# Kernel tuning notes

Measured on AMD Instinct MI355X. Metric: run time of the kernel, lower is better.

## Reference

```python
import jax, jax.numpy as jnp
import numpy as np

N = 50000
E = 800000
IN_CH = 128
HID = 64
HEADS = 4
EPS = 1e-5
NEG_SLOPE = 0.2


def _gat_conv(x, src, dst, W, a_src, a_dst, b, heads, out_ch, concat):
    n = x.shape[0]
    h = (x @ W).reshape(n, heads, out_ch)                      # [N,H,C]
    alpha_src = jnp.sum(h * a_src, axis=-1)                    # [N,H]
    alpha_dst = jnp.sum(h * a_dst, axis=-1)                    # [N,H]
    e = jax.nn.leaky_relu(alpha_src[src] + alpha_dst[dst], NEG_SLOPE)  # [E',H]
    # segment softmax over incoming edges of each destination node
    m = jax.ops.segment_max(e, dst, num_segments=n)            # [N,H]
    e = jnp.exp(e - m[dst])
    denom = jax.ops.segment_sum(e, dst, num_segments=n)        # [N,H]
    alpha = e / denom[dst]                                     # [E',H]
    msg = h[src] * alpha[:, :, None]                           # [E',H,C]
    out = jax.ops.segment_sum(msg, dst, num_segments=n)        # [N,H,C]
    if concat:
        out = out.reshape(n, heads * out_ch)
    else:
        out = out.mean(axis=1)
    return out + b


def _bn_eval(x, gamma, beta, mean, var):
    return (x - mean) * (gamma / jnp.sqrt(var + EPS)) + beta


def setup_inputs() -> dict:
    key = jax.random.key(0)
    ks = jax.random.split(key, 24)
    s = 0.1
    x = jax.random.normal(ks[0], (N, IN_CH), dtype=jnp.float32)
    edge_index = jax.random.randint(ks[1], (2, E), 0, N, dtype=jnp.int32)
    d0, d1 = IN_CH, HID * HEADS
    inp = {
        'x': x, 'edge_index': edge_index,
        # layer 0: in_ch -> hidden, heads=4, concat
        'W0': jax.random.normal(ks[2], (d0, HEADS * HID), jnp.float32) * s,
        'as0': jax.random.normal(ks[3], (HEADS, HID), jnp.float32) * s,
        'ad0': jax.random.normal(ks[4], (HEADS, HID), jnp.float32) * s,
        'b0': jax.random.normal(ks[5], (HEADS * HID,), jnp.float32) * s,
        # layer 1: hidden*heads -> hidden, heads=4, concat
        'W1': jax.random.normal(ks[6], (d1, HEADS * HID), jnp.float32) * s,
        'as1': jax.random.normal(ks[7], (HEADS, HID), jnp.float32) * s,
        'ad1': jax.random.normal(ks[8], (HEADS, HID), jnp.float32) * s,
        'b1': jax.random.normal(ks[9], (HEADS * HID,), jnp.float32) * s,
        # layer 2: hidden*heads -> 1, heads=1, no concat
        'W2': jax.random.normal(ks[10], (d1, 1), jnp.float32) * s,
        'as2': jax.random.normal(ks[11], (1, 1), jnp.float32) * s,
        'ad2': jax.random.normal(ks[12], (1, 1), jnp.float32) * s,
        'b2': jax.random.normal(ks[13], (1,), jnp.float32) * s,
        # batchnorm (eval) params for the two hidden layers
        'g0': jnp.ones((d1,), jnp.float32),
        'be0': jnp.zeros((d1,), jnp.float32),
        'm0': jax.random.normal(ks[14], (d1,), jnp.float32) * s,
        'v0': jnp.ones((d1,), jnp.float32),
        'g1': jnp.ones((d1,), jnp.float32),
        'be1': jnp.zeros((d1,), jnp.float32),
        'm1': jax.random.normal(ks[15], (d1,), jnp.float32) * s,
        'v1': jnp.ones((d1,), jnp.float32),
    }
    return inp


def reference(x, edge_index, W0, as0, ad0, b0, W1, as1, ad1, b1,
              W2, as2, ad2, b2, g0, be0, m0, v0, g1, be1, m1, v1):
    n = x.shape[0]
    loops = jnp.arange(n, dtype=edge_index.dtype)
    src = jnp.concatenate([edge_index[0], loops])  # add self-loops (PyG default)
    dst = jnp.concatenate([edge_index[1], loops])

    # layer 0 (no residual: shapes differ)
    h = _gat_conv(x, src, dst, W0, as0, ad0, b0, HEADS, HID, True)
    h = jax.nn.elu(_bn_eval(h, g0, be0, m0, v0))

    # layer 1 (residual: shapes match)
    res = h
    h = _gat_conv(h, src, dst, W1, as1, ad1, b1, HEADS, HID, True)
    h = jax.nn.elu(_bn_eval(h, g1, be1, m1, v1)) + res

    # output layer: heads=1, concat=False -> [N,1]
    out = _gat_conv(h, src, dst, W2, as2, ad2, b2, 1, 1, False)
    return out.squeeze(-1)
```

## Files before the change

### kernel.cpp

```cpp
#include <hip/hip_runtime.h>
#include <math.h>

#define NEG_SLOPE 0.2f
#define BN_EPS 1e-5f

typedef __attribute__((ext_vector_type(8))) short bf16x8;
typedef __attribute__((ext_vector_type(4))) float f32x4;

static __device__ __forceinline__ unsigned short f2bf(float f){
    unsigned u = __float_as_uint(f);
    u += 0x7FFFu + ((u >> 16) & 1u);
    return (unsigned short)(u >> 16);
}
static __device__ __forceinline__ float bf2f(unsigned short v){
    return __uint_as_float((unsigned)v << 16);
}

static __device__ __forceinline__ void gload_lds16(const void* g, void* l){
    __builtin_amdgcn_global_load_lds(
        (const __attribute__((address_space(1))) void*)g,
        (__attribute__((address_space(3))) void*)l, 16, 0, 0);
}

__global__ void conv_hilo_kernel(const float* __restrict__ x,
                                 unsigned short* __restrict__ hi,
                                 unsigned short* __restrict__ lo, int n4)
{
    int i = blockIdx.x * 256 + threadIdx.x;
    if (i >= n4) return;
    const float4 v = ((const float4*)x)[i];
    ushort4 h4, l4;
    h4.x = f2bf(v.x); l4.x = f2bf(v.x - bf2f(h4.x));
    h4.y = f2bf(v.y); l4.y = f2bf(v.y - bf2f(h4.y));
    h4.z = f2bf(v.z); l4.z = f2bf(v.z - bf2f(h4.z));
    h4.w = f2bf(v.w); l4.w = f2bf(v.w - bf2f(h4.w));
    ((ushort4*)hi)[i] = h4; ((ushort4*)lo)[i] = l4;
}

__global__ void repack_w_kernel(const float* __restrict__ W,
                                unsigned short* __restrict__ wbhi,
                                unsigned short* __restrict__ wblo)
{
    const int o = blockIdx.x * 256 + threadIdx.x;
    const int j = o & 7, ln = (o >> 3) & 63, ct = (o >> 9) & 15, kt = o >> 13;
    const int k = kt * 32 + 8 * (ln >> 4) + j;
    const int col = ct * 16 + (ln & 15);
    const float v = W[k * 256 + col];
    const unsigned short hb = f2bf(v);
    wbhi[o] = hb; wblo[o] = f2bf(v - bf2f(hb));
}

template<int K>
__global__ __launch_bounds__(256) void mfma_gemm_alpha(
    const unsigned short* __restrict__ xhi, const unsigned short* __restrict__ xlo,
    const unsigned short* __restrict__ wbhi, const unsigned short* __restrict__ wblo,
    const float* __restrict__ a_s, const float* __restrict__ a_d,
    unsigned short* __restrict__ hout,
    float* __restrict__ asrc, float* __restrict__ adst, int N)
{
    __shared__ unsigned short xa[8][512];
    __shared__ unsigned short wb[32][512];
    const int t = threadIdx.x, lane = t & 63, wid = t >> 6;
    const int n0 = blockIdx.x * 64;

    f32x4 acc[4][4];
#pragma unroll
    for (int rt = 0; rt < 4; ++rt)
#pragma unroll
        for (int q = 0; q < 4; ++q) acc[rt][q] = (f32x4){0.f, 0.f, 0.f, 0.f};

    for (int kt = 0; kt < K / 32; ++kt){
        __syncthreads();
#pragma unroll
        for (int ii = 0; ii < 2; ++ii){
            const int i = wid * 2 + ii;
            const int rt = i >> 1, plane = i & 1;
            int node = n0 + rt * 16 + (lane & 15);
            if (node > N - 1) node = N - 1;
            const unsigned short* src = (plane ? xlo : xhi)
                + (size_t)node * K + kt * 32 + 8 * (lane >> 4);
            gload_lds16(src, &xa[i][0]);
        }
#pragma unroll
        for (int ii = 0; ii < 8; ++ii){
            const int i = wid * 8 + ii;
            const int ct = i >> 1, plane = i & 1;
            const unsigned short* base = plane ? wblo : wbhi;
            gload_lds16(base + ((size_t)(kt * 16 + ct) * 64 + lane) * 8, &wb[i][0]);
        }
        __syncthreads();

        bf16x8 a[4][2];
#pragma unroll
        for (int rt = 0; rt < 4; ++rt)
#pragma unroll
            for (int pl = 0; pl < 2; ++pl)
                a[rt][pl] = *(const bf16x8*)&xa[rt * 2 + pl][lane * 8];

#pragma unroll
        for (int q = 0; q < 4; ++q){
            const int cti = wid * 4 + q;
            const bf16x8 bhi = *(const bf16x8*)&wb[cti * 2 + 0][lane * 8];
            const bf16x8 blo = *(const bf16x8*)&wb[cti * 2 + 1][lane * 8];
#pragma unroll
            for (int rt = 0; rt < 4; ++rt){
                acc[rt][q] = __builtin_amdgcn_mfma_f32_16x16x32_bf16(a[rt][0], bhi, acc[rt][q], 0, 0, 0);
                acc[rt][q] = __builtin_amdgcn_mfma_f32_16x16x32_bf16(a[rt][1], bhi, acc[rt][q], 0, 0, 0);
                acc[rt][q] = __builtin_amdgcn_mfma_f32_16x16x32_bf16(a[rt][0], blo, acc[rt][q], 0, 0, 0);
            }
        }
    }

    const int l15 = lane & 15, lg = lane >> 4;
    float avs[4], avd[4];
#pragma unroll
    for (int q = 0; q < 4; ++q){
        avs[q] = a_s[wid * 64 + q * 16 + l15];
        avd[q] = a_d[wid * 64 + q * 16 + l15];
    }
    float sp[4][4], dp[4][4];
#pragma unroll
    for (int rt = 0; rt < 4; ++rt){
#pragma unroll
        for (int reg = 0; reg < 4; ++reg){
            const int node = n0 + rt * 16 + lg * 4 + reg;
            float s = 0.f, d = 0.f;
            unsigned short hv[4];
#pragma unroll
            for (int q = 0; q < 4; ++q){
                const float v = acc[rt][q][reg];
                s = fmaf(v, avs[q], s); d = fmaf(v, avd[q], d);
                hv[q] = f2bf(v);
            }
            if (node < N){
#pragma unroll
                for (int q = 0; q < 4; ++q)
                    hout[(size_t)node * 256 + (wid * 4 + q) * 16 + l15] = hv[q];
            }
            sp[rt][reg] = s; dp[rt][reg] = d;
        }
    }
#pragma unroll
    for (int off = 1; off <= 8; off <<= 1){
#pragma unroll
        for (int rt = 0; rt < 4; ++rt)
#pragma unroll
            for (int reg = 0; reg < 4; ++reg){
                sp[rt][reg] += __shfl_xor(sp[rt][reg], off, 64);
                dp[rt][reg] += __shfl_xor(dp[rt][reg], off, 64);
            }
    }
    if (l15 == 0){
#pragma unroll
        for (int rt = 0; rt < 4; ++rt)
#pragma unroll
            for (int reg = 0; reg < 4; ++reg){
                const int node = n0 + rt * 16 + lg * 4 + reg;
                if (node < N){
                    asrc[(size_t)node * 4 + wid] = sp[rt][reg];
                    adst[(size_t)node * 4 + wid] = dp[rt][reg];
                }
            }
    }
}

__global__ void deg_init_kernel(int* __restrict__ deg, int N){
    int i = blockIdx.x * blockDim.x + threadIdx.x;
    if (i < N) deg[i] = 1;
}

__global__ void deg_hist_kernel(const int* __restrict__ ei, int E, int* __restrict__ deg){
    int e = blockIdx.x * blockDim.x + threadIdx.x;
    if (e < E) atomicAdd(&deg[ei[E + e]], 1);
}

__global__ __launch_bounds__(256) void part_sum_kernel(const int* __restrict__ deg,
                                                       int* __restrict__ bsum, int N)
{
    __shared__ int red[256];
    const int t = threadIdx.x;
    const int i0 = blockIdx.x * 1024 + t * 4;
    int s = 0;
    if (i0 + 3 < N){
        const int4 v = *(const int4*)&deg[i0];
        s = v.x + v.y + v.z + v.w;
    } else {
#pragma unroll
        for (int j = 0; j < 4; ++j) if (i0 + j < N) s += deg[i0 + j];
    }
    red[t] = s; __syncthreads();
    for (int off = 128; off >= 1; off >>= 1){
        if (t < off) red[t] += red[t + off];
        __syncthreads();
    }
    if (t == 0) bsum[blockIdx.x] = red[0];
}

__global__ __launch_bounds__(256) void scan_part_kernel(int* __restrict__ bsum, int nb,
                                                        int* __restrict__ row, int N)
{
    __shared__ int sh[256];
    const int t = threadIdx.x;
    const int v = (t < nb) ? bsum[t] : 0;
    sh[t] = v; __syncthreads();
    for (int off = 1; off < 256; off <<= 1){
        int u = (t >= off) ? sh[t - off] : 0;
        __syncthreads();
        sh[t] += u;
        __syncthreads();
    }
    if (t < nb) bsum[t] = sh[t] - v;
    if (t == nb - 1) row[N] = sh[t];
}

__global__ __launch_bounds__(256) void distribute_kernel(const int* __restrict__ deg,
    const int* __restrict__ bsum, int* __restrict__ row, int* __restrict__ cursor, int N)
{
    __shared__ int ts[256];
    const int t = threadIdx.x;
    const int i0 = blockIdx.x * 1024 + t * 4;
    int d[4]; int s = 0;
#pragma unroll
    for (int j = 0; j < 4; ++j){ d[j] = (i0 + j < N) ? deg[i0 + j] : 0; s += d[j]; }
    ts[t] = s; __syncthreads();
    for (int off = 1; off < 256; off <<= 1){
        int u = (t >= off) ? ts[t - off] : 0;
        __syncthreads();
        ts[t] += u;
        __syncthreads();
    }
    int base = bsum[blockIdx.x] + ts[t] - s;
#pragma unroll
    for (int j = 0; j < 4; ++j){
        if (i0 + j < N){ row[i0 + j] = base; cursor[i0 + j] = base; base += d[j]; }
    }
}

__global__ void scatter_kernel(const int* __restrict__ ei, int E, int N,
                               int* __restrict__ cursor, int* __restrict__ csr)
{
    int e = blockIdx.x * blockDim.x + threadIdx.x;
    if (e >= E + N) return;
    int s, d;
    if (e < E){ s = ei[e]; d = ei[E + e]; } else { s = d = e - E; }
    int pos = atomicAdd(&cursor[d], 1);
    csr[pos] = s;
}

#define DEG_CAP 128
__global__ __launch_bounds__(256) void agg4_kernel(
    const int* __restrict__ row, const int* __restrict__ csr,
    const float* __restrict__ asrc, const float* __restrict__ adst,
    const unsigned short* __restrict__ h,
    const float* __restrict__ b, const float* __restrict__ g,
    const float* __restrict__ be, const float* __restrict__ mean,
    const float* __restrict__ var,
    const unsigned short* __restrict__ reshi, const unsigned short* __restrict__ reslo,
    unsigned short* __restrict__ outhi, unsigned short* __restrict__ outlo, int N)
{
    __shared__ float4 plds[4][DEG_CAP];
    __shared__ int    slds[4][DEG_CAP];
    const int wid = threadIdx.x >> 6, lane = threadIdx.x & 63;
    const int node = blockIdx.x * 4 + wid;
    if (node >= N) return;
    const int beg = row[node], end = row[node + 1];
    const int head = lane >> 4, l15 = lane & 15;

    const float4 ad = *(const float4*)&adst[(size_t)node * 4];

    float d0 = 0.f, d1 = 0.f, d2 = 0.f, d3 = 0.f;
    for (int i = beg + lane; i < end; i += 64){
        const int s = csr[i];
        const float4 as = *(const float4*)&asrc[(size_t)s * 4];
        float v0 = as.x + ad.x, v1 = as.y + ad.y, v2 = as.z + ad.z, v3 = as.w + ad.w;
        v0 = v0 > 0.f ? v0 : NEG_SLOPE * v0;
        v1 = v1 > 0.f ? v1 : NEG_SLOPE * v1;
        v2 = v2 > 0.f ? v2 : NEG_SLOPE * v2;
        v3 = v3 > 0.f ? v3 : NEG_SLOPE * v3;
        const float p0 = __expf(v0), p1 = __expf(v1);
        const float p2 = __expf(v2), p3 = __expf(v3);
        d0 += p0; d1 += p1; d2 += p2; d3 += p3;
        const int slot = i - beg;
        if (slot < DEG_CAP){
            plds[wid][slot] = make_float4(p0, p1, p2, p3);
            slds[wid][slot] = s;
        }
    }
    for (int off = 32; off >= 1; off >>= 1){
        d0 += __shfl_xor(d0, off, 64); d1 += __shfl_xor(d1, off, 64);
        d2 += __shfl_xor(d2, off, 64); d3 += __shfl_xor(d3, off, 64);
    }

    float a0 = 0.f, a1 = 0.f, a2 = 0.f, a3 = 0.f;
    const int deg = end - beg;
    const int degc = deg < DEG_CAP ? deg : DEG_CAP;
    const float* pbase = (const float*)&plds[wid][0];

#define EDGE_BODY(slot)                                                        \
    {                                                                          \
        const float p_ = pbase[(slot) * 4 + head];                             \
        const int s_ = slds[wid][slot];                                        \
        const ushort4 hv_ = *(const ushort4*)&h[(size_t)s_ * 256 + lane * 4];  \
        a0 = fmaf(p_, bf2f(hv_.x), a0); a1 = fmaf(p_, bf2f(hv_.y), a1);        \
        a2 = fmaf(p_, bf2f(hv_.z), a2); a3 = fmaf(p_, bf2f(hv_.w), a3);        \
    }

    int i = 0;
    for (; i + 4 <= degc; i += 4){
        EDGE_BODY(i); EDGE_BODY(i + 1); EDGE_BODY(i + 2); EDGE_BODY(i + 3);
    }
    for (; i < degc; ++i) EDGE_BODY(i);
#undef EDGE_BODY

    for (int jj = beg + DEG_CAP; jj < end; ++jj){
        const int s = csr[jj];
        const float4 as = *(const float4*)&asrc[(size_t)s * 4];
        float e0 = as.x + ad.x, e1 = as.y + ad.y, e2 = as.z + ad.z, e3 = as.w + ad.w;
        float eh = (head == 0) ? e0 : (head == 1) ? e1 : (head == 2) ? e2 : e3;
        eh = eh > 0.f ? eh : NEG_SLOPE * eh;
        const float p = __expf(eh);
        const ushort4 hv = *(const ushort4*)&h[(size_t)s * 256 + lane * 4];
        a0 = fmaf(p, bf2f(hv.x), a0); a1 = fmaf(p, bf2f(hv.y), a1);
        a2 = fmaf(p, bf2f(hv.z), a2); a3 = fmaf(p, bf2f(hv.w), a3);
    }

    const float dsel = (head == 0) ? d0 : (head == 1) ? d1 : (head == 2) ? d2 : d3;
    const float rdi = 1.f / dsel;
    const int c0 = head * 64 + 4 * l15;
    const float4 bv  = *(const float4*)&b[c0];
    const float4 gv  = *(const float4*)&g[c0];
    const float4 bev = *(const float4*)&be[c0];
    const float4 mv  = *(const float4*)&mean[c0];
    const float4 vv4 = *(const float4*)&var[c0];
    const float ava[4]  = {a0, a1, a2, a3};
    const float bva[4]  = {bv.x, bv.y, bv.z, bv.w};
    const float gva[4]  = {gv.x, gv.y, gv.z, gv.w};
    const float beva[4] = {bev.x, bev.y, bev.z, bev.w};
    const float mva[4]  = {mv.x, mv.y, mv.z, mv.w};
    const float vva[4]  = {vv4.x, vv4.y, vv4.z, vv4.w};
    float rh[4] = {0.f, 0.f, 0.f, 0.f};
    if (reshi){
        const ushort4 r1 = *(const ushort4*)&reshi[(size_t)node * 256 + c0];
        const ushort4 r2 = *(const ushort4*)&reslo[(size_t)node * 256 + c0];
        rh[0] = bf2f(r1.x) + bf2f(r2.x); rh[1] = bf2f(r1.y) + bf2f(r2.y);
        rh[2] = bf2f(r1.z) + bf2f(r2.z); rh[3] = bf2f(r1.w) + bf2f(r2.w);
    }
    unsigned short hos[4], los[4];
#pragma unroll
    for (int j = 0; j < 4; ++j){
        float vvv = ava[j] * rdi + bva[j];
        vvv = (vvv - mva[j]) * (gva[j] * rsqrtf(vva[j] + BN_EPS)) + beva[j];
        vvv = vvv > 0.f ? vvv : (__expf(vvv) - 1.f);
        vvv += rh[j];
        const unsigned short hb = f2bf(vvv);
        hos[j] = hb; los[j] = f2bf(vvv - bf2f(hb));
    }
    ushort4 ho, lo4;
    ho.x = hos[0];  ho.y = hos[1];  ho.z = hos[2];  ho.w = hos[3];
    lo4.x = los[0]; lo4.y = los[1]; lo4.z = los[2]; lo4.w = los[3];
    *(ushort4*)&outhi[(size_t)node * 256 + c0] = ho;
    *(ushort4*)&outlo[(size_t)node * 256 + c0] = lo4;
}

__global__ __launch_bounds__(256) void gemm2_kernel(
    const unsigned short* __restrict__ xhi, const unsigned short* __restrict__ xlo,
    const float* __restrict__ W2, float* __restrict__ h2, int N)
{
    const int wid = threadIdx.x >> 6, lane = threadIdx.x & 63;
    const int n = blockIdx.x * 4 + wid;
    if (n >= N) return;
    float sum = 0.f;
#pragma unroll
    for (int i = 0; i < 4; ++i){
        const int c = i * 64 + lane;
        sum += (bf2f(xhi[(size_t)n * 256 + c]) + bf2f(xlo[(size_t)n * 256 + c])) * W2[c];
    }
    for (int off = 32; off >= 1; off >>= 1) sum += __shfl_xor(sum, off, 64);
    if (lane == 0) h2[n] = sum;
}

__global__ void agg2_kernel(const int* __restrict__ row, const int* __restrict__ csr,
                            const float* __restrict__ h2,
                            const float* __restrict__ as2, const float* __restrict__ ad2,
                            const float* __restrict__ b2, float* __restrict__ out, int N)
{
    const int n = blockIdx.x * blockDim.x + threadIdx.x;
    if (n >= N) return;
    const float A_s = as2[0];
    const float hd  = h2[n] * ad2[0];
    const int beg = row[n], end = row[n + 1];
    float den = 0.f, acc = 0.f;
    for (int i = beg; i < end; ++i){
        const float hv = h2[csr[i]];
        float a = fmaf(A_s, hv, hd);
        a = a > 0.f ? a : NEG_SLOPE * a;
        const float p = __expf(a);
        den += p; acc = fmaf(p, hv, acc);
    }
    out[n] = acc / den + b2[0];
}

extern "C" void kernel_launch(void* const* d_in, const int* in_sizes, int n_in,
                              void* d_out, int out_size, void* d_ws, size_t ws_size,
                              hipStream_t stream)
{
    const float* x   = (const float*)d_in[0];
    const int*   ei  = (const int*)  d_in[1];
    const float* W0  = (const float*)d_in[2];
    const float* as0 = (const float*)d_in[3];
    const float* ad0 = (const float*)d_in[4];
    const float* b0  = (const float*)d_in[5];
    const float* W1  = (const float*)d_in[6];
    const float* as1 = (const float*)d_in[7];
    const float* ad1 = (const float*)d_in[8];
    const float* b1  = (const float*)d_in[9];
    const float* W2  = (const float*)d_in[10];
    const float* as2 = (const float*)d_in[11];
    const float* ad2 = (const float*)d_in[12];
    const float* b2  = (const float*)d_in[13];
    const float* g0  = (const float*)d_in[14];
    const float* be0 = (const float*)d_in[15];
    const float* m0  = (const float*)d_in[16];
    const float* v0  = (const float*)d_in[17];
    const float* g1  = (const float*)d_in[18];
    const float* be1 = (const float*)d_in[19];
    const float* m1  = (const float*)d_in[20];
    const float* v1  = (const float*)d_in[21];

    const int N = in_sizes[0] / 128;
    const int E = in_sizes[1] / 2;
    const int EN = E + N;

    char* w = (char*)d_ws;
    unsigned short* H    = (unsigned short*)w;  w += (size_t)N * 256 * 2;
    unsigned short* X0hi = (unsigned short*)w;
    unsigned short* X0lo = X0hi + (size_t)N * 128;
    unsigned short* P1hi = X0hi;
    w += (size_t)N * 256 * 2;
    unsigned short* P0hi = (unsigned short*)w;  w += (size_t)N * 256 * 2;
    unsigned short* P0lo = (unsigned short*)w;  w += (size_t)N * 256 * 2;
    unsigned short* P1lo = (unsigned short*)w;  w += (size_t)N * 256 * 2;
    float*    asrc   = (float*)w;   w += (size_t)N * 4 * 4;
    float*    adst   = (float*)w;   w += (size_t)N * 4 * 4;
    int*      deg    = (int*)w;     w += (size_t)N * 4;
    int*      cursor = (int*)w;     w += (size_t)N * 4;
    int*      csr    = (int*)w;     w += (size_t)EN * 4;
    float*    h2     = (float*)w;   w += (size_t)N * 4;
    int*      bsum   = (int*)w;     w += 1024;
    unsigned short* Wb0hi = (unsigned short*)w; w += (size_t)128 * 256 * 2;
    unsigned short* Wb0lo = (unsigned short*)w; w += (size_t)128 * 256 * 2;
    unsigned short* Wb1hi = (unsigned short*)w; w += (size_t)256 * 256 * 2;
    unsigned short* Wb1lo = (unsigned short*)w; w += (size_t)256 * 256 * 2;
    int*      rowp   = (int*)w;     w += (size_t)(N + 1) * 4;

    const int gN64  = (N + 63) / 64;
    const int gN4   = (N + 3) / 4;
    const int gNt   = (N + 255) / 256;
    const int gE    = (E + 255) / 256;
    const int gEN   = (EN + 255) / 256;
    const int nb    = (N + 1023) / 1024;

    conv_hilo_kernel<<<(N * 128 / 4 + 255) / 256, 256, 0, stream>>>(x, X0hi, X0lo, N * 128 / 4);
    repack_w_kernel<<<128, 256, 0, stream>>>(W0, Wb0hi, Wb0lo);
    repack_w_kernel<<<256, 256, 0, stream>>>(W1, Wb1hi, Wb1lo);
    deg_init_kernel<<<gNt, 256, 0, stream>>>(deg, N);
    deg_hist_kernel<<<gE, 256, 0, stream>>>(ei, E, deg);
    part_sum_kernel<<<nb, 256, 0, stream>>>(deg, bsum, N);
    scan_part_kernel<<<1, 256, 0, stream>>>(bsum, nb, rowp, N);
    distribute_kernel<<<nb, 256, 0, stream>>>(deg, bsum, rowp, cursor, N);
    scatter_kernel<<<gEN, 256, 0, stream>>>(ei, E, N, cursor, csr);

    mfma_gemm_alpha<128><<<gN64, 256, 0, stream>>>(X0hi, X0lo, Wb0hi, Wb0lo,
                                                   as0, ad0, H, asrc, adst, N);
    agg4_kernel<<<gN4, 256, 0, stream>>>(rowp, csr, asrc, adst, H,
                                         b0, g0, be0, m0, v0,
                                         nullptr, nullptr, P0hi, P0lo, N);

    mfma_gemm_alpha<256><<<gN64, 256, 0, stream>>>(P0hi, P0lo, Wb1hi, Wb1lo,
                                                   as1, ad1, H, asrc, adst, N);
    agg4_kernel<<<gN4, 256, 0, stream>>>(rowp, csr, asrc, adst, H,
                                         b1, g1, be1, m1, v1,
                                         P0hi, P0lo, P1hi, P1lo, N);

    gemm2_kernel<<<gN4, 256, 0, stream>>>(P1hi, P1lo, W2, h2, N);
    agg2_kernel<<<gNt, 256, 0, stream>>>(rowp, csr, h2, as2, ad2, b2, (float*)d_out, N);
}
```

Measured before the change: 339.5 us.

## Store GAT features head-major and split aggregation into per-head blocks

The GEMM epilogue now writes the bf16 feature matrix as [head][node][64] instead of [node][256]. The aggregation kernel launches four times as many blocks, one per head, so each wavefront handles one (node, head) pair. It processes four edges at once across 16-lane subgroups and combines them with cross-lane shuffles. The aim is more parallelism and a per-head working set small enough to stay in cache during the random gathers. In exchange, CSR reading and the softmax logits are recomputed for every head, and only 16 lanes do the epilogue.

Result: slower. 458.1 us (+34.9%).

```diff
diff --git a/kernel.cpp b/kernel.cpp
--- a/kernel.cpp
+++ b/kernel.cpp
@@ -135,7 +135,7 @@
             if (node < N){
 #pragma unroll
                 for (int q = 0; q < 4; ++q)
-                    hout[(size_t)node * 256 + (wid * 4 + q) * 16 + l15] = hv[q];
+                    hout[((size_t)wid * N + node) * 64 + q * 16 + l15] = hv[q];
             }
             sp[rt][reg] = s; dp[rt][reg] = d;
         }
@@ -248,118 +248,103 @@
 }
 
 #define DEG_CAP 128
-__global__ __launch_bounds__(256) void agg4_kernel(
+__global__ __launch_bounds__(256) void agg4h_kernel(
     const int* __restrict__ row, const int* __restrict__ csr,
     const float* __restrict__ asrc, const float* __restrict__ adst,
-    const unsigned short* __restrict__ h,
+    const unsigned short* __restrict__ hh,
     const float* __restrict__ b, const float* __restrict__ g,
     const float* __restrict__ be, const float* __restrict__ mean,
     const float* __restrict__ var,
     const unsigned short* __restrict__ reshi, const unsigned short* __restrict__ reslo,
-    unsigned short* __restrict__ outhi, unsigned short* __restrict__ outlo, int N)
-{
-    __shared__ float4 plds[4][DEG_CAP];
-    __shared__ int    slds[4][DEG_CAP];
+    unsigned short* __restrict__ outhi, unsigned short* __restrict__ outlo,
+    int N, int gN4)
+{
+    __shared__ float plds[4][DEG_CAP];
+    __shared__ int   slds[4][DEG_CAP];
     const int wid = threadIdx.x >> 6, lane = threadIdx.x & 63;
-    const int node = blockIdx.x * 4 + wid;
+    const int head = blockIdx.x / gN4;
+    const int node = (blockIdx.x - head * gN4) * 4 + wid;
     if (node >= N) return;
-    const int beg = row[node], end = row[node + 1];
-    const int head = lane >> 4, l15 = lane & 15;
-
-    const float4 ad = *(const float4*)&adst[(size_t)node * 4];
-
-    float d0 = 0.f, d1 = 0.f, d2 = 0.f, d3 = 0.f;
-    for (int i = beg + lane; i < end; i += 64){
-        const int s = csr[i];
-        const float4 as = *(const float4*)&asrc[(size_t)s * 4];
-        float v0 = as.x + ad.x, v1 = as.y + ad.y, v2 = as.z + ad.z, v3 = as.w + ad.w;
-        v0 = v0 > 0.f ? v0 : NEG_SLOPE * v0;
-        v1 = v1 > 0.f ? v1 : NEG_SLOPE * v1;
-        v2 = v2 > 0.f ? v2 : NEG_SLOPE * v2;
-        v3 = v3 > 0.f ? v3 : NEG_SLOPE * v3;
-        const float p0 = __expf(v0), p1 = __expf(v1);
-        const float p2 = __expf(v2), p3 = __expf(v3);
-        d0 += p0; d1 += p1; d2 += p2; d3 += p3;
-        const int slot = i - beg;
-        if (slot < DEG_CAP){
-            plds[wid][slot] = make_float4(p0, p1, p2, p3);
-            slds[wid][slot] = s;
-        }
-    }
-    for (int off = 32; off >= 1; off >>= 1){
-        d0 += __shfl_xor(d0, off, 64); d1 += __shfl_xor(d1, off, 64);
-        d2 += __shfl_xor(d2, off, 64); d3 += __shfl_xor(d3, off, 64);
-    }
-
+    const int beg = row[node], end = row[node + 1], deg = end - beg;
+    const float adh = adst[(size_t)node * 4 + head];
+
+    float den = 0.f;
+    for (int i = lane; i < deg; i += 64){
+        const int s = csr[beg + i];
+        float v = asrc[(size_t)s * 4 + head] + adh;
+        v = v > 0.f ? v : NEG_SLOPE * v;
+        const float p = __expf(v);
+        den += p;
+        if (i < DEG_CAP){ plds[wid][i] = p; slds[wid][i] = s; }
+    }
+    for (int off = 32; off >= 1; off >>= 1) den += __shfl_xor(den, off, 64);
+
+    const int sub = lane >> 4, l15 = lane & 15;
+    const int degc = deg < DEG_CAP ? deg : DEG_CAP;
+    const size_t hbase = (size_t)head * N;
     float a0 = 0.f, a1 = 0.f, a2 = 0.f, a3 = 0.f;
-    const int deg = end - beg;
-    const int degc = deg < DEG_CAP ? deg : DEG_CAP;
-    const float* pbase = (const float*)&plds[wid][0];
-
-#define EDGE_BODY(slot)                                                        \
-    {                                                                          \
-        const float p_ = pbase[(slot) * 4 + head];                             \
-        const int s_ = slds[wid][slot];                                        \
-        const ushort4 hv_ = *(const ushort4*)&h[(size_t)s_ * 256 + lane * 4];  \
-        a0 = fmaf(p_, bf2f(hv_.x), a0); a1 = fmaf(p_, bf2f(hv_.y), a1);        \
-        a2 = fmaf(p_, bf2f(hv_.z), a2); a3 = fmaf(p_, bf2f(hv_.w), a3);        \
-    }
-
-    int i = 0;
-    for (; i + 4 <= degc; i += 4){
-        EDGE_BODY(i); EDGE_BODY(i + 1); EDGE_BODY(i + 2); EDGE_BODY(i + 3);
-    }
-    for (; i < degc; ++i) EDGE_BODY(i);
-#undef EDGE_BODY
-
-    for (int jj = beg + DEG_CAP; jj < end; ++jj){
-        const int s = csr[jj];
-        const float4 as = *(const float4*)&asrc[(size_t)s * 4];
-        float e0 = as.x + ad.x, e1 = as.y + ad.y, e2 = as.z + ad.z, e3 = as.w + ad.w;
-        float eh = (head == 0) ? e0 : (head == 1) ? e1 : (head == 2) ? e2 : e3;
-        eh = eh > 0.f ? eh : NEG_SLOPE * eh;
-        const float p = __expf(eh);
-        const ushort4 hv = *(const ushort4*)&h[(size_t)s * 256 + lane * 4];
-        a0 = fmaf(p, bf2f(hv.x), a0); a1 = fmaf(p, bf2f(hv.y), a1);
-        a2 = fmaf(p, bf2f(hv.z), a2); a3 = fmaf(p, bf2f(hv.w), a3);
-    }
-
-    const float dsel = (head == 0) ? d0 : (head == 1) ? d1 : (head == 2) ? d2 : d3;
-    const float rdi = 1.f / dsel;
-    const int c0 = head * 64 + 4 * l15;
-    const float4 bv  = *(const float4*)&b[c0];
-    const float4 gv  = *(const float4*)&g[c0];
-    const float4 bev = *(const float4*)&be[c0];
-    const float4 mv  = *(const float4*)&mean[c0];
-    const float4 vv4 = *(const float4*)&var[c0];
-    const float ava[4]  = {a0, a1, a2, a3};
-    const float bva[4]  = {bv.x, bv.y, bv.z, bv.w};
-    const float gva[4]  = {gv.x, gv.y, gv.z, gv.w};
-    const float beva[4] = {bev.x, bev.y, bev.z, bev.w};
-    const float mva[4]  = {mv.x, mv.y, mv.z, mv.w};
-    const float vva[4]  = {vv4.x, vv4.y, vv4.z, vv4.w};
-    float rh[4] = {0.f, 0.f, 0.f, 0.f};
-    if (reshi){
-        const ushort4 r1 = *(const ushort4*)&reshi[(size_t)node * 256 + c0];
-        const ushort4 r2 = *(const ushort4*)&reslo[(size_t)node * 256 + c0];
-        rh[0] = bf2f(r1.x) + bf2f(r2.x); rh[1] = bf2f(r1.y) + bf2f(r2.y);
-        rh[2] = bf2f(r1.z) + bf2f(r2.z); rh[3] = bf2f(r1.w) + bf2f(r2.w);
-    }
-    unsigned short hos[4], los[4];
-#pragma unroll
-    for (int j = 0; j < 4; ++j){
-        float vvv = ava[j] * rdi + bva[j];
-        vvv = (vvv - mva[j]) * (gva[j] * rsqrtf(vva[j] + BN_EPS)) + beva[j];
-        vvv = vvv > 0.f ? vvv : (__expf(vvv) - 1.f);
-        vvv += rh[j];
-        const unsigned short hb = f2bf(vvv);
-        hos[j] = hb; los[j] = f2bf(vvv - bf2f(hb));
-    }
-    ushort4 ho, lo4;
-    ho.x = hos[0];  ho.y = hos[1];  ho.z = hos[2];  ho.w = hos[3];
-    lo4.x = los[0]; lo4.y = los[1]; lo4.z = los[2]; lo4.w = los[3];
-    *(ushort4*)&outhi[(size_t)node * 256 + c0] = ho;
-    *(ushort4*)&outlo[(size_t)node * 256 + c0] = lo4;
+    for (int i = 0; i < degc; i += 4){
+        const int it = i + sub;
+        const bool ok = it < degc;
+        const int s_  = slds[wid][ok ? it : 0];
+        const float p_ = ok ? plds[wid][it] : 0.f;
+        const ushort4 hv = *(const ushort4*)&hh[(hbase + s_) * 64 + 4 * l15];
+        a0 = fmaf(p_, bf2f(hv.x), a0); a1 = fmaf(p_, bf2f(hv.y), a1);
+        a2 = fmaf(p_, bf2f(hv.z), a2); a3 = fmaf(p_, bf2f(hv.w), a3);
+    }
+    if (sub == 0){
+        for (int j = beg + DEG_CAP; j < end; ++j){
+            const int s = csr[j];
+            float v = asrc[(size_t)s * 4 + head] + adh;
+            v = v > 0.f ? v : NEG_SLOPE * v;
+            const float p = __expf(v);
+            const ushort4 hv = *(const ushort4*)&hh[(hbase + s) * 64 + 4 * l15];
+            a0 = fmaf(p, bf2f(hv.x), a0); a1 = fmaf(p, bf2f(hv.y), a1);
+            a2 = fmaf(p, bf2f(hv.z), a2); a3 = fmaf(p, bf2f(hv.w), a3);
+        }
+    }
+    a0 += __shfl_xor(a0, 16, 64); a0 += __shfl_xor(a0, 32, 64);
+    a1 += __shfl_xor(a1, 16, 64); a1 += __shfl_xor(a1, 32, 64);
+    a2 += __shfl_xor(a2, 16, 64); a2 += __shfl_xor(a2, 32, 64);
+    a3 += __shfl_xor(a3, 16, 64); a3 += __shfl_xor(a3, 32, 64);
+
+    if (lane < 16){
+        const float rdi = 1.f / den;
+        const int c0 = head * 64 + 4 * lane;
+        const float4 bv  = *(const float4*)&b[c0];
+        const float4 gv  = *(const float4*)&g[c0];
+        const float4 bev = *(const float4*)&be[c0];
+        const float4 mv  = *(const float4*)&mean[c0];
+        const float4 vv4 = *(const float4*)&var[c0];
+        float rh[4] = {0.f, 0.f, 0.f, 0.f};
+        if (reshi){
+            const ushort4 r1 = *(const ushort4*)&reshi[(size_t)node * 256 + c0];
+            const ushort4 r2 = *(const ushort4*)&reslo[(size_t)node * 256 + c0];
+            rh[0] = bf2f(r1.x) + bf2f(r2.x); rh[1] = bf2f(r1.y) + bf2f(r2.y);
+            rh[2] = bf2f(r1.z) + bf2f(r2.z); rh[3] = bf2f(r1.w) + bf2f(r2.w);
+        }
+        const float ava[4]  = {a0, a1, a2, a3};
+        const float bva[4]  = {bv.x, bv.y, bv.z, bv.w};
+        const float gva[4]  = {gv.x, gv.y, gv.z, gv.w};
+        const float beva[4] = {bev.x, bev.y, bev.z, bev.w};
+        const float mva[4]  = {mv.x, mv.y, mv.z, mv.w};
+        const float vva[4]  = {vv4.x, vv4.y, vv4.z, vv4.w};
+        unsigned short hos[4], los[4];
+#pragma unroll
+        for (int j = 0; j < 4; ++j){
+            float vvv = ava[j] * rdi + bva[j];
+            vvv = (vvv - mva[j]) * (gva[j] * rsqrtf(vva[j] + BN_EPS)) + beva[j];
+            vvv = vvv > 0.f ? vvv : (__expf(vvv) - 1.f);
+            vvv += rh[j];
+            const unsigned short hb = f2bf(vvv);
+            hos[j] = hb; los[j] = f2bf(vvv - bf2f(hb));
+        }
+        ushort4 ho, lo4;
+        ho.x = hos[0];  ho.y = hos[1];  ho.z = hos[2];  ho.w = hos[3];
+        lo4.x = los[0]; lo4.y = los[1]; lo4.z = los[2]; lo4.w = los[3];
+        *(ushort4*)&outhi[(size_t)node * 256 + c0] = ho;
+        *(ushort4*)&outlo[(size_t)node * 256 + c0] = lo4;
+    }
 }
 
 __global__ __launch_bounds__(256) void gemm2_kernel(
@@ -472,15 +457,15 @@
 
     mfma_gemm_alpha<128><<<gN64, 256, 0, stream>>>(X0hi, X0lo, Wb0hi, Wb0lo,
                                                    as0, ad0, H, asrc, adst, N);
-    agg4_kernel<<<gN4, 256, 0, stream>>>(rowp, csr, asrc, adst, H,
-                                         b0, g0, be0, m0, v0,
-                                         nullptr, nullptr, P0hi, P0lo, N);
+    agg4h_kernel<<<gN4 * 4, 256, 0, stream>>>(rowp, csr, asrc, adst, H,
+                                              b0, g0, be0, m0, v0,
+                                              nullptr, nullptr, P0hi, P0lo, N, gN4);
 
     mfma_gemm_alpha<256><<<gN64, 256, 0, stream>>>(P0hi, P0lo, Wb1hi, Wb1lo,
                                                    as1, ad1, H, asrc, adst, N);
-    agg4_kernel<<<gN4, 256, 0, stream>>>(rowp, csr, asrc, adst, H,
-                                         b1, g1, be1, m1, v1,
-                                         P0hi, P0lo, P1hi, P1lo, N);
+    agg4h_kernel<<<gN4 * 4, 256, 0, stream>>>(rowp, csr, asrc, adst, H,
+                                              b1, g1, be1, m1, v1,
+                                              P0hi, P0lo, P1hi, P1lo, N, gN4);
 
     gemm2_kernel<<<gN4, 256, 0, stream>>>(P1hi, P1lo, W2, h2, N);
     agg2_kernel<<<gNt, 256, 0, stream>>>(rowp, csr, h2, as2, ad2, b2, (float*)d_out, N);
```
